# Kernel optimization log

Hardware: AMD Instinct MI355X
Metric: run time of the kernel (lower is better)

## Reference

```python
import jax, jax.numpy as jnp
import numpy as np
from jax import lax


def _sobel3d_kernels():
    # Standard separable 3D Sobel: derivative d=[-1,0,1] along one axis,
    # smoothing s=[1,2,1] along the other two. Axes order (D, H, W).
    d = np.array([-1.0, 0.0, 1.0], dtype=np.float32)
    s = np.array([1.0, 2.0, 1.0], dtype=np.float32)
    kx = np.einsum('i,j,k->ijk', d, s, s)  # derivative along D
    ky = np.einsum('i,j,k->ijk', s, d, s)  # derivative along H
    kz = np.einsum('i,j,k->ijk', s, s, d)  # derivative along W
    # Stack as [Cout=3, Cin=1, 3, 3, 3] -> one conv computes x,y,z grads at once.
    return jnp.asarray(np.stack([kx, ky, kz])[:, None])


_DN = ('NCDHW', 'OIDHW', 'NCDHW')


def _conv3(x, k):
    # x: [N, 1, D, H, W], k: [3, 1, 3, 3, 3] -> [N, 3, D-2, H-2, W-2]
    # torch F.conv3d and lax conv are both cross-correlation; VALID padding.
    return lax.conv_general_dilated(x, k, (1, 1, 1), 'VALID', dimension_numbers=_DN)


def _g2(inp, k):
    # inp: [B, D, H, W, C] (channels last, as the torch module permutes)
    b, dd, hh, ww, c = inp.shape
    x = jnp.transpose(inp, (0, 4, 1, 2, 3)).reshape(b * c, 1, dd, hh, ww)
    g1 = _conv3(x, k)                                  # [B*C, 3, D-2, H-2, W-2]
    mag = jnp.sqrt(jnp.sum(g1 * g1, axis=1, keepdims=True))  # first-order magnitude
    g2 = _conv3(mag, k)                                # [B*C, 3, D-4, H-4, W-4]
    gx, gy, gz = g2[:, 0], g2[:, 1], g2[:, 2]
    # Faithful to source: sqrt(x^2 + y^2) + z^2 (note: z is squared, not inside sqrt)
    out = jnp.sqrt(gx * gx + gy * gy) + gz * gz        # [B*C, D-4, H-4, W-4]
    return out.reshape(b, c, *out.shape[1:])


def setup_inputs() -> dict:
    key = jax.random.key(0)
    k1, k2 = jax.random.split(key)
    pred = jax.random.normal(k1, (2, 64, 64, 64, 32), dtype=jnp.float32)
    hr = jax.random.normal(k2, (2, 64, 64, 64, 32), dtype=jnp.float32)
    return {'pred': pred, 'hr': hr}


def reference(pred, hr):
    k = _sobel3d_kernels()
    return jnp.mean(jnp.abs(_g2(pred, k) - _g2(hr, k)))
```

## Files before the change

### kernel.cpp

```cpp
#include <hip/hip_runtime.h>
#include <hip/hip_fp16.h>


constexpr int BDIM = 256;
constexpr size_t IN_B = 8388608;
constexpr int IN_D = 131072;
constexpr int IN_H = 2048;
constexpr int M = 62;
constexpr int F = 60;
constexpr int C = 32;
constexpr int MROW = M * C;
constexpr size_t MAGSZ = (size_t)M * M * MROW;
constexpr size_t PLANE = (size_t)M * MROW;
constexpr unsigned NPART = 1440;

__device__ __forceinline__ float4 ld4(const float* p) {
    return *reinterpret_cast<const float4*>(p);
}
__device__ __forceinline__ float2 ldh2(const __half* p) {
    return __half22float2(*reinterpret_cast<const __half2*>(p));
}
__device__ __forceinline__ float4 sm3(float4 a, float4 b, float4 c) {
    return make_float4(a.x + 2.f * b.x + c.x, a.y + 2.f * b.y + c.y,
                       a.z + 2.f * b.z + c.z, a.w + 2.f * b.w + c.w);
}
__device__ __forceinline__ float4 df2(float4 a, float4 c) {
    return make_float4(c.x - a.x, c.y - a.y, c.z - a.z, c.w - a.w);
}

struct P1W { float4 A[2], B[2], C[2]; };

__device__ __forceinline__ void p1_plane(const float* __restrict__ col, size_t zoff,
                                         P1W& W)
{
    float4 S[4], D[4];
#pragma unroll
    for (int r = 0; r < 4; ++r) {
        const float* p = col + zoff + (size_t)r * IN_H;
        float4 a = ld4(p), b = ld4(p + C), c = ld4(p + 2 * C);
        S[r] = sm3(a, b, c);
        D[r] = df2(a, c);
    }
#pragma unroll
    for (int k = 0; k < 2; ++k) {
        W.A[k] = sm3(S[k], S[k+1], S[k+2]);
        W.B[k] = df2(S[k], S[k+2]);
        W.C[k] = sm3(D[k], D[k+1], D[k+2]);
    }
}

__device__ __forceinline__ void p1_emit(const P1W& W0, const P1W& W1, const P1W& W2,
                                        __half* __restrict__ mag, size_t cb,
                                        int z, int y0, bool wr)
{
    if (!wr) return;
#pragma unroll
    for (int k = 0; k < 2; ++k) {
        float4 gx = df2(W0.A[k], W2.A[k]);
        float4 gy = sm3(W0.B[k], W1.B[k], W2.B[k]);
        float4 gz = sm3(W0.C[k], W1.C[k], W2.C[k]);
        float mx = sqrtf(gx.x * gx.x + gy.x * gy.x + gz.x * gz.x);
        float my = sqrtf(gx.y * gx.y + gy.y * gy.y + gz.y * gz.y);
        float mz = sqrtf(gx.z * gx.z + gy.z * gy.z + gz.z * gz.z);
        float mw = sqrtf(gx.w * gx.w + gy.w * gy.w + gz.w * gz.w);
        union { __half2 h[2]; float2 f; } u;
        u.h[0] = __floats2half2_rn(mx, my);
        u.h[1] = __floats2half2_rn(mz, mw);
        *reinterpret_cast<float2*>(mag + ((size_t)z * M + (y0 + k)) * MROW + cb)
            = u.f;
    }
}

__global__ __launch_bounds__(BDIM) void sobel_mag_v7(
    const float* __restrict__ pred, const float* __restrict__ hr,
    __half* __restrict__ magP, __half* __restrict__ magH,
    int b, unsigned* __restrict__ counter, int zeroCtr)
{
    if (zeroCtr && blockIdx.x == 0 && blockIdx.y == 0 && blockIdx.z == 0 &&
        threadIdx.x == 0)
        __hip_atomic_store(counter, 0u, __ATOMIC_RELAXED,
                           __HIP_MEMORY_SCOPE_AGENT);

    const int xt = blockIdx.x & 1, yt = blockIdx.x >> 1;
    const int zc = blockIdx.y;
    const float* __restrict__ in  = blockIdx.z ? hr   : pred;
    __half*      __restrict__ mag = blockIdx.z ? magH : magP;

    const int c4 = (threadIdx.x & 7) << 2;
    const int xl = threadIdx.x >> 3;
    const int x0 = xt * 30;
    const int x  = x0 + xl;
    const bool wr = (xt == 0) || (xl >= 2);
    const int y0 = yt * 2;
    const int z0 = zc * 8;
    const int zn = min(8, M - z0);

    const float* col = in + (size_t)b * IN_B + (size_t)y0 * IN_H
                          + (size_t)x * C + c4;
    const size_t cb = (size_t)x * C + c4;

    P1W W0, W1, W2;
    p1_plane(col, (size_t)(z0 + 0) * IN_D, W0);
    p1_plane(col, (size_t)(z0 + 1) * IN_D, W1);
    int z = 0;
    while (true) {
        p1_plane(col, (size_t)(z0 + z + 2) * IN_D, W2);
        p1_emit(W0, W1, W2, mag, cb, z0 + z, y0, wr);
        if (++z >= zn) break;
        p1_plane(col, (size_t)(z0 + z + 2) * IN_D, W0);
        p1_emit(W1, W2, W0, mag, cb, z0 + z, y0, wr);
        if (++z >= zn) break;
        p1_plane(col, (size_t)(z0 + z + 2) * IN_D, W1);
        p1_emit(W2, W0, W1, mag, cb, z0 + z, y0, wr);
        if (++z >= zn) break;
    }
}

struct P2W { float2 A[2], B[2], C[2]; };

__device__ __forceinline__ void p2_plane(const __half* __restrict__ col, size_t zoff,
                                         P2W& W)
{
    float2 SX[4], DX[4];
#pragma unroll
    for (int j = 0; j < 4; ++j) {
        const __half* p = col + zoff + (size_t)j * MROW;
        float2 a = ldh2(p), b = ldh2(p + C), c = ldh2(p + 2 * C);
        SX[j] = make_float2(a.x + 2.f * b.x + c.x, a.y + 2.f * b.y + c.y);
        DX[j] = make_float2(c.x - a.x, c.y - a.y);
    }
#pragma unroll
    for (int k = 0; k < 2; ++k) {
        W.A[k] = make_float2(SX[k].x + 2.f * SX[k+1].x + SX[k+2].x,
                             SX[k].y + 2.f * SX[k+1].y + SX[k+2].y);
        W.B[k] = make_float2(SX[k+2].x - SX[k].x, SX[k+2].y - SX[k].y);
        W.C[k] = make_float2(DX[k].x + 2.f * DX[k+1].x + DX[k+2].x,
                             DX[k].y + 2.f * DX[k+1].y + DX[k+2].y);
    }
}

__device__ __forceinline__ void p2_emit(const P2W& P0, const P2W& P1, const P2W& P2,
                                        const P2W& H0, const P2W& H1, const P2W& H2,
                                        float& acc)
{
#pragma unroll
    for (int k = 0; k < 2; ++k) {
        float gxPx = P2.A[k].x - P0.A[k].x;
        float gxPy = P2.A[k].y - P0.A[k].y;
        float gyPx = P0.B[k].x + 2.f * P1.B[k].x + P2.B[k].x;
        float gyPy = P0.B[k].y + 2.f * P1.B[k].y + P2.B[k].y;
        float gzPx = P0.C[k].x + 2.f * P1.C[k].x + P2.C[k].x;
        float gzPy = P0.C[k].y + 2.f * P1.C[k].y + P2.C[k].y;
        float gxHx = H2.A[k].x - H0.A[k].x;
        float gxHy = H2.A[k].y - H0.A[k].y;
        float gyHx = H0.B[k].x + 2.f * H1.B[k].x + H2.B[k].x;
        float gyHy = H0.B[k].y + 2.f * H1.B[k].y + H2.B[k].y;
        float gzHx = H0.C[k].x + 2.f * H1.C[k].x + H2.C[k].x;
        float gzHy = H0.C[k].y + 2.f * H1.C[k].y + H2.C[k].y;
        float oPx = sqrtf(gxPx * gxPx + gyPx * gyPx) + gzPx * gzPx;
        float oPy = sqrtf(gxPy * gxPy + gyPy * gyPy) + gzPy * gzPy;
        float oHx = sqrtf(gxHx * gxHx + gyHx * gyHx) + gzHx * gzHx;
        float oHy = sqrtf(gxHy * gxHy + gyHy * gyHy) + gzHy * gzHy;
        acc += fabsf(oPx - oHx) + fabsf(oPy - oHy);
    }
}

__global__ __launch_bounds__(BDIM) void sobel2_v7(
    const __half* __restrict__ magP, const __half* __restrict__ magH,
    int b, float* __restrict__ partial, unsigned* __restrict__ counter,
    float* __restrict__ out)
{
    const int xt = blockIdx.x & 3, yt = blockIdx.x >> 2;
    const int zc = blockIdx.y;
    const int y0 = yt * 2;
    const int z0 = zc * 10;
    const int xraw = xt * 16 + (threadIdx.x >> 4);
    const bool xok = xraw < F;
    const int x = min(xraw, F - 1);
    const int c2 = (threadIdx.x & 15) << 1;

    const size_t colo = (size_t)y0 * MROW + (size_t)x * C + c2;
    const __half* colP = magP + colo;
    const __half* colH = magH + colo;

    P2W P0, P1, P2, H0, H1, H2;
    p2_plane(colP, (size_t)(z0 + 0) * PLANE, P0);
    p2_plane(colH, (size_t)(z0 + 0) * PLANE, H0);
    p2_plane(colP, (size_t)(z0 + 1) * PLANE, P1);
    p2_plane(colH, (size_t)(z0 + 1) * PLANE, H1);
    float acc = 0.f;
    int z = 0;
    while (true) {
        p2_plane(colP, (size_t)(z0 + z + 2) * PLANE, P2);
        p2_plane(colH, (size_t)(z0 + z + 2) * PLANE, H2);
        if (xok) p2_emit(P0, P1, P2, H0, H1, H2, acc);
        if (++z >= 10) break;
        p2_plane(colP, (size_t)(z0 + z + 2) * PLANE, P0);
        p2_plane(colH, (size_t)(z0 + z + 2) * PLANE, H0);
        if (xok) p2_emit(P1, P2, P0, H1, H2, H0, acc);
        if (++z >= 10) break;
        p2_plane(colP, (size_t)(z0 + z + 2) * PLANE, P1);
        p2_plane(colH, (size_t)(z0 + z + 2) * PLANE, H1);
        if (xok) p2_emit(P2, P0, P1, H2, H0, H1, acc);
        if (++z >= 10) break;
    }

    for (int o = 32; o > 0; o >>= 1) acc += __shfl_down(acc, o, 64);
    __shared__ float sred[BDIM / 64];
    __shared__ int isLast;
    const int lane = threadIdx.x & 63, wv = threadIdx.x >> 6;
    if (lane == 0) sred[wv] = acc;
    __syncthreads();
    if (threadIdx.x == 0) {
        float t = 0.f;
#pragma unroll
        for (int i = 0; i < BDIM / 64; ++i) t += sred[i];
        const size_t pidx = (size_t)b * 720 + (size_t)zc * 120 + blockIdx.x;
        __hip_atomic_store(&partial[pidx], t, __ATOMIC_RELAXED,
                           __HIP_MEMORY_SCOPE_AGENT);
        const unsigned old = __hip_atomic_fetch_add(counter, 1u, __ATOMIC_ACQ_REL,
                                                    __HIP_MEMORY_SCOPE_AGENT);
        isLast = (old == NPART - 1u) ? 1 : 0;
    }
    __syncthreads();

    if (isLast) {
        double a = 0.0;
        for (unsigned i = threadIdx.x; i < NPART; i += BDIM)
            a += (double)__hip_atomic_load(&partial[i], __ATOMIC_RELAXED,
                                           __HIP_MEMORY_SCOPE_AGENT);
        for (int o = 32; o > 0; o >>= 1) a += __shfl_down(a, o, 64);
        __shared__ double sd[BDIM / 64];
        if (lane == 0) sd[wv] = a;
        __syncthreads();
        if (threadIdx.x == 0) {
            double t = 0.0;
#pragma unroll
            for (int i = 0; i < BDIM / 64; ++i) t += sd[i];
            out[0] = (float)(t / 13824000.0);
        }
    }
}

extern "C" void kernel_launch(void* const* d_in, const int* in_sizes, int n_in,
                              void* d_out, int out_size, void* d_ws, size_t ws_size,
                              hipStream_t stream)
{
    const float* pred = (const float*)d_in[0];
    const float* hr   = (const float*)d_in[1];

    float* partial = (float*)d_ws;
    unsigned* counter = (unsigned*)((char*)d_ws + 32768);
    __half* magP = (__half*)((char*)d_ws + 65536);
    __half* magH = magP + MAGSZ;

    for (int b = 0; b < 2; ++b) {
        sobel_mag_v7<<<dim3(62, 8, 2), BDIM, 0, stream>>>(
            pred, hr, magP, magH, b, counter, b == 0 ? 1 : 0);
        sobel2_v7<<<dim3(120, 6), BDIM, 0, stream>>>(
            magP, magH, b, partial, counter, (float*)d_out);
    }
}
```

Before: 257.5 us.

## Stage input planes through LDS with async global_load_lds double buffering

Both stencil kernels now stream each z-plane into shared memory with asynchronous global-to-LDS DMA loads, double-buffered and fenced by explicit vmcnt waits and barriers. Threads then read their neighbouring x values from LDS instead of issuing overlapping global loads. The magnitude buffer gets a padded row pitch, the first kernel covers a full x row per block, and the second kernel switches to 4-wide half vectors with a new grid shape and partial count. This aims to cut redundant global traffic and hide load latency, at the cost of 64KB of LDS per block in the first kernel (lowering occupancy) and hand-tuned wait counts that are easy to get wrong.

```diff
diff --git a/kernel.cpp b/kernel.cpp
--- a/kernel.cpp
+++ b/kernel.cpp
@@ -8,17 +8,38 @@
 constexpr int IN_H = 2048;
 constexpr int M = 62;
 constexpr int F = 60;
-constexpr int C = 32;
-constexpr int MROW = M * C;
-constexpr size_t MAGSZ = (size_t)M * M * MROW;
-constexpr size_t PLANE = (size_t)M * MROW;
-constexpr unsigned NPART = 1440;
+constexpr int PMROW = 2048;
+constexpr size_t PPLANE = (size_t)M * PMROW;
+constexpr size_t PMAGSZ = (size_t)M * PPLANE;
+constexpr unsigned NPART = 1800;
+
+__device__ __forceinline__ void dma16(const void* g, void* l) {
+    __builtin_amdgcn_global_load_lds(
+        (const __attribute__((address_space(1))) void*)g,
+        (__attribute__((address_space(3))) void*)l, 16, 0, 0);
+}
+
+#define WAITBAR(N) do { \
+    asm volatile("s_waitcnt vmcnt(" #N ")" ::: "memory"); \
+    __builtin_amdgcn_sched_barrier(0); \
+    __builtin_amdgcn_s_barrier(); \
+    __builtin_amdgcn_sched_barrier(0); \
+} while (0)
+
+#define MIDBAR() do { \
+    __builtin_amdgcn_sched_barrier(0); \
+    __builtin_amdgcn_s_barrier(); \
+    __builtin_amdgcn_sched_barrier(0); \
+} while (0)
 
 __device__ __forceinline__ float4 ld4(const float* p) {
     return *reinterpret_cast<const float4*>(p);
 }
-__device__ __forceinline__ float2 ldh2(const __half* p) {
-    return __half22float2(*reinterpret_cast<const __half2*>(p));
+__device__ __forceinline__ float4 ldh4(const __half* p) {
+    float2 r = *reinterpret_cast<const float2*>(p);
+    const __half2* h = reinterpret_cast<const __half2*>(&r);
+    float2 lo = __half22float2(h[0]), hi = __half22float2(h[1]);
+    return make_float4(lo.x, lo.y, hi.x, hi.y);
 }
 __device__ __forceinline__ float4 sm3(float4 a, float4 b, float4 c) {
     return make_float4(a.x + 2.f * b.x + c.x, a.y + 2.f * b.y + c.y,
@@ -30,14 +51,14 @@
 
 struct P1W { float4 A[2], B[2], C[2]; };
 
-__device__ __forceinline__ void p1_plane(const float* __restrict__ col, size_t zoff,
-                                         P1W& W)
+__device__ __forceinline__ void p1_partials(const float* __restrict__ sb,
+                                            int x, int c4, P1W& W)
 {
     float4 S[4], D[4];
 #pragma unroll
     for (int r = 0; r < 4; ++r) {
-        const float* p = col + zoff + (size_t)r * IN_H;
-        float4 a = ld4(p), b = ld4(p + C), c = ld4(p + 2 * C);
+        const float* p = sb + r * 2048 + x * 32 + c4;
+        float4 a = ld4(p), b = ld4(p + 32), c = ld4(p + 64);
         S[r] = sm3(a, b, c);
         D[r] = df2(a, c);
     }
@@ -49,191 +70,246 @@
     }
 }
 
-__device__ __forceinline__ void p1_emit(const P1W& W0, const P1W& W1, const P1W& W2,
-                                        __half* __restrict__ mag, size_t cb,
-                                        int z, int y0, bool wr)
-{
-    if (!wr) return;
+__device__ __forceinline__ void p1_emit4(const P1W& W0, const P1W& W1, const P1W& W2,
+                                         __half* __restrict__ mag, int x, int c4,
+                                         int z, int y0)
+{
 #pragma unroll
     for (int k = 0; k < 2; ++k) {
         float4 gx = df2(W0.A[k], W2.A[k]);
         float4 gy = sm3(W0.B[k], W1.B[k], W2.B[k]);
         float4 gz = sm3(W0.C[k], W1.C[k], W2.C[k]);
-        float mx = sqrtf(gx.x * gx.x + gy.x * gy.x + gz.x * gz.x);
-        float my = sqrtf(gx.y * gx.y + gy.y * gy.y + gz.y * gz.y);
-        float mz = sqrtf(gx.z * gx.z + gy.z * gy.z + gz.z * gz.z);
-        float mw = sqrtf(gx.w * gx.w + gy.w * gy.w + gz.w * gz.w);
+        float m0 = sqrtf(gx.x * gx.x + gy.x * gy.x + gz.x * gz.x);
+        float m1 = sqrtf(gx.y * gx.y + gy.y * gy.y + gz.y * gz.y);
+        float m2 = sqrtf(gx.z * gx.z + gy.z * gy.z + gz.z * gz.z);
+        float m3 = sqrtf(gx.w * gx.w + gy.w * gy.w + gz.w * gz.w);
         union { __half2 h[2]; float2 f; } u;
-        u.h[0] = __floats2half2_rn(mx, my);
-        u.h[1] = __floats2half2_rn(mz, mw);
-        *reinterpret_cast<float2*>(mag + ((size_t)z * M + (y0 + k)) * MROW + cb)
-            = u.f;
-    }
-}
-
-__global__ __launch_bounds__(BDIM) void sobel_mag_v7(
+        u.h[0] = __floats2half2_rn(m0, m1);
+        u.h[1] = __floats2half2_rn(m2, m3);
+        *reinterpret_cast<float2*>(
+            mag + (size_t)z * PPLANE + (size_t)(y0 + k) * PMROW + x * 32 + c4) = u.f;
+    }
+}
+
+__global__ __launch_bounds__(BDIM) void sobel_mag_v8(
     const float* __restrict__ pred, const float* __restrict__ hr,
     __half* __restrict__ magP, __half* __restrict__ magH,
     int b, unsigned* __restrict__ counter, int zeroCtr)
 {
+    __shared__ char smem[65536];
+
     if (zeroCtr && blockIdx.x == 0 && blockIdx.y == 0 && blockIdx.z == 0 &&
         threadIdx.x == 0)
         __hip_atomic_store(counter, 0u, __ATOMIC_RELAXED,
                            __HIP_MEMORY_SCOPE_AGENT);
 
-    const int xt = blockIdx.x & 1, yt = blockIdx.x >> 1;
+    const int yt = blockIdx.x;
     const int zc = blockIdx.y;
     const float* __restrict__ in  = blockIdx.z ? hr   : pred;
     __half*      __restrict__ mag = blockIdx.z ? magH : magP;
-
-    const int c4 = (threadIdx.x & 7) << 2;
-    const int xl = threadIdx.x >> 3;
-    const int x0 = xt * 30;
-    const int x  = x0 + xl;
-    const bool wr = (xt == 0) || (xl >= 2);
     const int y0 = yt * 2;
     const int z0 = zc * 8;
     const int zn = min(8, M - z0);
-
-    const float* col = in + (size_t)b * IN_B + (size_t)y0 * IN_H
-                          + (size_t)x * C + c4;
-    const size_t cb = (size_t)x * C + c4;
-
-    P1W W0, W1, W2;
-    p1_plane(col, (size_t)(z0 + 0) * IN_D, W0);
-    p1_plane(col, (size_t)(z0 + 1) * IN_D, W1);
+    const int tid = threadIdx.x;
+    const int c4 = (tid & 7) << 2;
+    const int xA = tid >> 3;
+    const int xB = xA + 32;
+    const bool xBok = xB < M;
+
+    const char* gIn = (const char*)in +
+        ((size_t)b * IN_B + (size_t)y0 * IN_H) * 4 + (size_t)tid * 16;
+
+    auto ISSUE = [&](int q, int zz) {
+        const char* g = gIn + (size_t)min(zz, 63) * (IN_D * 4);
+        char* l = smem + q * 32768 + tid * 16;
+#pragma unroll
+        for (int k = 0; k < 8; ++k)
+            dma16(g + k * 4096, l + k * 4096);
+    };
+
+    P1W A0, A1, A2, B0, B1, B2;
+    auto COMPA = [&](int q, P1W& Wa, P1W& Wb) {
+        const float* sb = (const float*)(smem + q * 32768);
+        p1_partials(sb, xA, c4, Wa);
+        if (xBok) p1_partials(sb, xB, c4, Wb);
+    };
+
+    ISSUE(0, z0 + 0); ISSUE(1, z0 + 1);
+    WAITBAR(8);
+    COMPA(0, A0, B0);
+    MIDBAR(); ISSUE(0, z0 + 2);
+    WAITBAR(8);
+    COMPA(1, A1, B1);
+    MIDBAR(); ISSUE(1, z0 + 3);
+
     int z = 0;
     while (true) {
-        p1_plane(col, (size_t)(z0 + z + 2) * IN_D, W2);
-        p1_emit(W0, W1, W2, mag, cb, z0 + z, y0, wr);
+        WAITBAR(8);
+        COMPA(z & 1, A2, B2);
+        p1_emit4(A0, A1, A2, mag, xA, c4, z0 + z, y0);
+        if (xBok) p1_emit4(B0, B1, B2, mag, xB, c4, z0 + z, y0);
+        MIDBAR(); ISSUE(z & 1, z0 + z + 4);
         if (++z >= zn) break;
-        p1_plane(col, (size_t)(z0 + z + 2) * IN_D, W0);
-        p1_emit(W1, W2, W0, mag, cb, z0 + z, y0, wr);
+        WAITBAR(8);
+        COMPA(z & 1, A0, B0);
+        p1_emit4(A1, A2, A0, mag, xA, c4, z0 + z, y0);
+        if (xBok) p1_emit4(B1, B2, B0, mag, xB, c4, z0 + z, y0);
+        MIDBAR(); ISSUE(z & 1, z0 + z + 4);
         if (++z >= zn) break;
-        p1_plane(col, (size_t)(z0 + z + 2) * IN_D, W1);
-        p1_emit(W2, W0, W1, mag, cb, z0 + z, y0, wr);
+        WAITBAR(8);
+        COMPA(z & 1, A1, B1);
+        p1_emit4(A2, A0, A1, mag, xA, c4, z0 + z, y0);
+        if (xBok) p1_emit4(B2, B0, B1, mag, xB, c4, z0 + z, y0);
+        MIDBAR(); ISSUE(z & 1, z0 + z + 4);
         if (++z >= zn) break;
     }
-}
-
-struct P2W { float2 A[2], B[2], C[2]; };
-
-__device__ __forceinline__ void p2_plane(const __half* __restrict__ col, size_t zoff,
-                                         P2W& W)
-{
-    float2 SX[4], DX[4];
+    asm volatile("s_waitcnt vmcnt(0)" ::: "memory");
+}
+
+struct P2W4 { float4 A[2], B[2], C[2]; };
+
+__device__ __forceinline__ void p2_partials(const __half* __restrict__ sb,
+                                            int xl, int c4, P2W4& W)
+{
+    float4 S[4], D[4];
 #pragma unroll
     for (int j = 0; j < 4; ++j) {
-        const __half* p = col + zoff + (size_t)j * MROW;
-        float2 a = ldh2(p), b = ldh2(p + C), c = ldh2(p + 2 * C);
-        SX[j] = make_float2(a.x + 2.f * b.x + c.x, a.y + 2.f * b.y + c.y);
-        DX[j] = make_float2(c.x - a.x, c.y - a.y);
+        const __half* p = sb + j * 1024 + xl * 32 + c4;
+        float4 a = ldh4(p), b = ldh4(p + 32), c = ldh4(p + 64);
+        S[j] = sm3(a, b, c);
+        D[j] = df2(a, c);
     }
 #pragma unroll
     for (int k = 0; k < 2; ++k) {
-        W.A[k] = make_float2(SX[k].x + 2.f * SX[k+1].x + SX[k+2].x,
-                             SX[k].y + 2.f * SX[k+1].y + SX[k+2].y);
-        W.B[k] = make_float2(SX[k+2].x - SX[k].x, SX[k+2].y - SX[k].y);
-        W.C[k] = make_float2(DX[k].x + 2.f * DX[k+1].x + DX[k+2].x,
-                             DX[k].y + 2.f * DX[k+1].y + DX[k+2].y);
-    }
-}
-
-__device__ __forceinline__ void p2_emit(const P2W& P0, const P2W& P1, const P2W& P2,
-                                        const P2W& H0, const P2W& H1, const P2W& H2,
-                                        float& acc)
+        W.A[k] = sm3(S[k], S[k+1], S[k+2]);
+        W.B[k] = df2(S[k], S[k+2]);
+        W.C[k] = sm3(D[k], D[k+1], D[k+2]);
+    }
+}
+
+__device__ __forceinline__ void p2_emit4(const P2W4& P0, const P2W4& P1, const P2W4& P2,
+                                         const P2W4& H0, const P2W4& H1, const P2W4& H2,
+                                         float& acc)
 {
 #pragma unroll
     for (int k = 0; k < 2; ++k) {
-        float gxPx = P2.A[k].x - P0.A[k].x;
-        float gxPy = P2.A[k].y - P0.A[k].y;
-        float gyPx = P0.B[k].x + 2.f * P1.B[k].x + P2.B[k].x;
-        float gyPy = P0.B[k].y + 2.f * P1.B[k].y + P2.B[k].y;
-        float gzPx = P0.C[k].x + 2.f * P1.C[k].x + P2.C[k].x;
-        float gzPy = P0.C[k].y + 2.f * P1.C[k].y + P2.C[k].y;
-        float gxHx = H2.A[k].x - H0.A[k].x;
-        float gxHy = H2.A[k].y - H0.A[k].y;
-        float gyHx = H0.B[k].x + 2.f * H1.B[k].x + H2.B[k].x;
-        float gyHy = H0.B[k].y + 2.f * H1.B[k].y + H2.B[k].y;
-        float gzHx = H0.C[k].x + 2.f * H1.C[k].x + H2.C[k].x;
-        float gzHy = H0.C[k].y + 2.f * H1.C[k].y + H2.C[k].y;
-        float oPx = sqrtf(gxPx * gxPx + gyPx * gyPx) + gzPx * gzPx;
-        float oPy = sqrtf(gxPy * gxPy + gyPy * gyPy) + gzPy * gzPy;
-        float oHx = sqrtf(gxHx * gxHx + gyHx * gyHx) + gzHx * gzHx;
-        float oHy = sqrtf(gxHy * gxHy + gyHy * gyHy) + gzHy * gzHy;
-        acc += fabsf(oPx - oHx) + fabsf(oPy - oHy);
-    }
-}
-
-__global__ __launch_bounds__(BDIM) void sobel2_v7(
+        float4 gxP = df2(P0.A[k], P2.A[k]);
+        float4 gyP = sm3(P0.B[k], P1.B[k], P2.B[k]);
+        float4 gzP = sm3(P0.C[k], P1.C[k], P2.C[k]);
+        float4 gxH = df2(H0.A[k], H2.A[k]);
+        float4 gyH = sm3(H0.B[k], H1.B[k], H2.B[k]);
+        float4 gzH = sm3(H0.C[k], H1.C[k], H2.C[k]);
+        acc += fabsf((sqrtf(gxP.x*gxP.x + gyP.x*gyP.x) + gzP.x*gzP.x)
+                   - (sqrtf(gxH.x*gxH.x + gyH.x*gyH.x) + gzH.x*gzH.x));
+        acc += fabsf((sqrtf(gxP.y*gxP.y + gyP.y*gyP.y) + gzP.y*gzP.y)
+                   - (sqrtf(gxH.y*gxH.y + gyH.y*gyH.y) + gzH.y*gzH.y));
+        acc += fabsf((sqrtf(gxP.z*gxP.z + gyP.z*gyP.z) + gzP.z*gzP.z)
+                   - (sqrtf(gxH.z*gxH.z + gyH.z*gyH.z) + gzH.z*gzH.z));
+        acc += fabsf((sqrtf(gxP.w*gxP.w + gyP.w*gyP.w) + gzP.w*gzP.w)
+                   - (sqrtf(gxH.w*gxH.w + gyH.w*gyH.w) + gzH.w*gzH.w));
+    }
+}
+
+__global__ __launch_bounds__(BDIM) void sobel2_v8(
     const __half* __restrict__ magP, const __half* __restrict__ magH,
     int b, float* __restrict__ partial, unsigned* __restrict__ counter,
     float* __restrict__ out)
 {
-    const int xt = blockIdx.x & 3, yt = blockIdx.x >> 2;
+    __shared__ char smem[32768];
+
+    const int xt = blockIdx.x & 1, yt = blockIdx.x >> 1;
     const int zc = blockIdx.y;
+    const int x0 = xt * 30;
     const int y0 = yt * 2;
-    const int z0 = zc * 10;
-    const int xraw = xt * 16 + (threadIdx.x >> 4);
-    const bool xok = xraw < F;
-    const int x = min(xraw, F - 1);
-    const int c2 = (threadIdx.x & 15) << 1;
-
-    const size_t colo = (size_t)y0 * MROW + (size_t)x * C + c2;
-    const __half* colP = magP + colo;
-    const __half* colH = magH + colo;
-
-    P2W P0, P1, P2, H0, H1, H2;
-    p2_plane(colP, (size_t)(z0 + 0) * PLANE, P0);
-    p2_plane(colH, (size_t)(z0 + 0) * PLANE, H0);
-    p2_plane(colP, (size_t)(z0 + 1) * PLANE, P1);
-    p2_plane(colH, (size_t)(z0 + 1) * PLANE, H1);
+    const int z0 = zc * 4;
+    const int tid = threadIdx.x;
+    const int c4 = (tid & 7) << 2;
+    const int xl = tid >> 3;
+    const bool xok = xl < 30;
+
+    const char* gPbase = (const char*)magP + (size_t)y0 * 4096 + (size_t)x0 * 64;
+    const char* gHbase = (const char*)magH + (size_t)y0 * 4096 + (size_t)x0 * 64;
+    const int sub = tid >> 7;
+    const int off = (tid & 127) * 16;
+
+    auto ISSUE = [&](int q, int zz) {
+        const size_t pb = (size_t)min(zz, M - 1) * (PPLANE * 2);
+        const char* gP = gPbase + pb;
+        const char* gH = gHbase + pb;
+        char* lb = smem + q * 16384;
+        const int j0 = sub, j1 = 2 + sub;
+        dma16(gP + (size_t)j0 * 4096 + off, lb + j0 * 2048 + off);
+        dma16(gP + (size_t)j1 * 4096 + off, lb + j1 * 2048 + off);
+        dma16(gH + (size_t)j0 * 4096 + off, lb + 8192 + j0 * 2048 + off);
+        dma16(gH + (size_t)j1 * 4096 + off, lb + 8192 + j1 * 2048 + off);
+    };
+
+    P2W4 P0, P1, P2, H0, H1, H2;
+    auto COMP = [&](int q, P2W4& P, P2W4& H) {
+        if (!xok) return;
+        const __half* sb = (const __half*)(smem + q * 16384);
+        p2_partials(sb,        xl, c4, P);
+        p2_partials(sb + 4096, xl, c4, H);
+    };
+
     float acc = 0.f;
-    int z = 0;
-    while (true) {
-        p2_plane(colP, (size_t)(z0 + z + 2) * PLANE, P2);
-        p2_plane(colH, (size_t)(z0 + z + 2) * PLANE, H2);
-        if (xok) p2_emit(P0, P1, P2, H0, H1, H2, acc);
-        if (++z >= 10) break;
-        p2_plane(colP, (size_t)(z0 + z + 2) * PLANE, P0);
-        p2_plane(colH, (size_t)(z0 + z + 2) * PLANE, H0);
-        if (xok) p2_emit(P1, P2, P0, H1, H2, H0, acc);
-        if (++z >= 10) break;
-        p2_plane(colP, (size_t)(z0 + z + 2) * PLANE, P1);
-        p2_plane(colH, (size_t)(z0 + z + 2) * PLANE, H1);
-        if (xok) p2_emit(P2, P0, P1, H2, H0, H1, acc);
-        if (++z >= 10) break;
-    }
+
+    ISSUE(0, z0 + 0); ISSUE(1, z0 + 1);
+    WAITBAR(4);
+    COMP(0, P0, H0);
+    MIDBAR(); ISSUE(0, z0 + 2);
+    WAITBAR(4);
+    COMP(1, P1, H1);
+    MIDBAR(); ISSUE(1, z0 + 3);
+
+    WAITBAR(4);
+    COMP(0, P2, H2);
+    if (xok) p2_emit4(P0, P1, P2, H0, H1, H2, acc);
+    MIDBAR(); ISSUE(0, z0 + 4);
+    WAITBAR(4);
+    COMP(1, P0, H0);
+    if (xok) p2_emit4(P1, P2, P0, H1, H2, H0, acc);
+    MIDBAR(); ISSUE(1, z0 + 5);
+    WAITBAR(4);
+    COMP(0, P1, H1);
+    if (xok) p2_emit4(P2, P0, P1, H2, H0, H1, acc);
+    MIDBAR(); ISSUE(0, z0 + 6);
+    WAITBAR(4);
+    COMP(1, P2, H2);
+    if (xok) p2_emit4(P0, P1, P2, H0, H1, H2, acc);
+
+    asm volatile("s_waitcnt vmcnt(0)" ::: "memory");
+    __syncthreads();
 
     for (int o = 32; o > 0; o >>= 1) acc += __shfl_down(acc, o, 64);
-    __shared__ float sred[BDIM / 64];
-    __shared__ int isLast;
-    const int lane = threadIdx.x & 63, wv = threadIdx.x >> 6;
+    float* sred = (float*)smem;
+    int* isLast = (int*)(smem + 64);
+    double* sd = (double*)(smem + 128);
+    const int lane = tid & 63, wv = tid >> 6;
     if (lane == 0) sred[wv] = acc;
     __syncthreads();
-    if (threadIdx.x == 0) {
+    if (tid == 0) {
         float t = 0.f;
 #pragma unroll
         for (int i = 0; i < BDIM / 64; ++i) t += sred[i];
-        const size_t pidx = (size_t)b * 720 + (size_t)zc * 120 + blockIdx.x;
+        const size_t pidx = (size_t)b * 900 + (size_t)zc * 60 + blockIdx.x;
         __hip_atomic_store(&partial[pidx], t, __ATOMIC_RELAXED,
                            __HIP_MEMORY_SCOPE_AGENT);
         const unsigned old = __hip_atomic_fetch_add(counter, 1u, __ATOMIC_ACQ_REL,
                                                     __HIP_MEMORY_SCOPE_AGENT);
-        isLast = (old == NPART - 1u) ? 1 : 0;
+        *isLast = (old == NPART - 1u) ? 1 : 0;
     }
     __syncthreads();
 
-    if (isLast) {
+    if (*isLast) {
         double a = 0.0;
-        for (unsigned i = threadIdx.x; i < NPART; i += BDIM)
+        for (unsigned i = tid; i < NPART; i += BDIM)
             a += (double)__hip_atomic_load(&partial[i], __ATOMIC_RELAXED,
                                            __HIP_MEMORY_SCOPE_AGENT);
         for (int o = 32; o > 0; o >>= 1) a += __shfl_down(a, o, 64);
-        __shared__ double sd[BDIM / 64];
         if (lane == 0) sd[wv] = a;
         __syncthreads();
-        if (threadIdx.x == 0) {
+        if (tid == 0) {
             double t = 0.0;
 #pragma unroll
             for (int i = 0; i < BDIM / 64; ++i) t += sd[i];
@@ -252,12 +328,12 @@
     float* partial = (float*)d_ws;
     unsigned* counter = (unsigned*)((char*)d_ws + 32768);
     __half* magP = (__half*)((char*)d_ws + 65536);
-    __half* magH = magP + MAGSZ;
+    __half* magH = magP + PMAGSZ;
 
     for (int b = 0; b < 2; ++b) {
-        sobel_mag_v7<<<dim3(62, 8, 2), BDIM, 0, stream>>>(
+        sobel_mag_v8<<<dim3(31, 8, 2), BDIM, 0, stream>>>(
             pred, hr, magP, magH, b, counter, b == 0 ? 1 : 0);
-        sobel2_v7<<<dim3(120, 6), BDIM, 0, stream>>>(
+        sobel2_v8<<<dim3(60, 15), BDIM, 0, stream>>>(
             magP, magH, b, partial, counter, (float*)d_out);
     }
 }
```

New measurement: 279.0 us. 1.08x slower.

## Fuse both Sobel passes into one persistent cooperative kernel with grid sync

Applied to the files above, without the earlier changes.

Replaces the four launches (two per batch) with a single cooperative kernel of 512 persistent blocks. Each block loops over first-pass work units for both batches, waits at a grid-wide sync, then loops over second-pass units, and ends with one final reduction. The aim is to cut launch gaps and let both batches run together, at the cost of a larger magnitude workspace and a grid barrier. The old multi-launch path is kept as a fallback if the workspace is too small or the cooperative launch fails.

```diff
diff --git a/kernel.cpp b/kernel.cpp
--- a/kernel.cpp
+++ b/kernel.cpp
@@ -1,8 +1,12 @@
 #include <hip/hip_runtime.h>
 #include <hip/hip_fp16.h>
+#include <hip/hip_cooperative_groups.h>
+
+namespace cg = cooperative_groups;
 
 
 constexpr int BDIM = 256;
+constexpr int NB   = 512;
 constexpr size_t IN_B = 8388608;
 constexpr int IN_D = 131072;
 constexpr int IN_H = 2048;
@@ -12,7 +16,6 @@
 constexpr int MROW = M * C;
 constexpr size_t MAGSZ = (size_t)M * M * MROW;
 constexpr size_t PLANE = (size_t)M * MROW;
-constexpr unsigned NPART = 1440;
 
 __device__ __forceinline__ float4 ld4(const float* p) {
     return *reinterpret_cast<const float4*>(p);
@@ -59,37 +62,26 @@
         float4 gx = df2(W0.A[k], W2.A[k]);
         float4 gy = sm3(W0.B[k], W1.B[k], W2.B[k]);
         float4 gz = sm3(W0.C[k], W1.C[k], W2.C[k]);
-        float mx = sqrtf(gx.x * gx.x + gy.x * gy.x + gz.x * gz.x);
-        float my = sqrtf(gx.y * gx.y + gy.y * gy.y + gz.y * gz.y);
-        float mz = sqrtf(gx.z * gx.z + gy.z * gy.z + gz.z * gz.z);
-        float mw = sqrtf(gx.w * gx.w + gy.w * gy.w + gz.w * gz.w);
+        float m0 = sqrtf(gx.x * gx.x + gy.x * gy.x + gz.x * gz.x);
+        float m1 = sqrtf(gx.y * gx.y + gy.y * gy.y + gz.y * gz.y);
+        float m2 = sqrtf(gx.z * gx.z + gy.z * gy.z + gz.z * gz.z);
+        float m3 = sqrtf(gx.w * gx.w + gy.w * gy.w + gz.w * gz.w);
         union { __half2 h[2]; float2 f; } u;
-        u.h[0] = __floats2half2_rn(mx, my);
-        u.h[1] = __floats2half2_rn(mz, mw);
+        u.h[0] = __floats2half2_rn(m0, m1);
+        u.h[1] = __floats2half2_rn(m2, m3);
         *reinterpret_cast<float2*>(mag + ((size_t)z * M + (y0 + k)) * MROW + cb)
             = u.f;
     }
 }
 
-__global__ __launch_bounds__(BDIM) void sobel_mag_v7(
-    const float* __restrict__ pred, const float* __restrict__ hr,
-    __half* __restrict__ magP, __half* __restrict__ magH,
-    int b, unsigned* __restrict__ counter, int zeroCtr)
-{
-    if (zeroCtr && blockIdx.x == 0 && blockIdx.y == 0 && blockIdx.z == 0 &&
-        threadIdx.x == 0)
-        __hip_atomic_store(counter, 0u, __ATOMIC_RELAXED,
-                           __HIP_MEMORY_SCOPE_AGENT);
-
-    const int xt = blockIdx.x & 1, yt = blockIdx.x >> 1;
-    const int zc = blockIdx.y;
-    const float* __restrict__ in  = blockIdx.z ? hr   : pred;
-    __half*      __restrict__ mag = blockIdx.z ? magH : magP;
-
-    const int c4 = (threadIdx.x & 7) << 2;
-    const int xl = threadIdx.x >> 3;
-    const int x0 = xt * 30;
-    const int x  = x0 + xl;
+__device__ __forceinline__ void p1_unit(const float* __restrict__ in,
+                                        __half* __restrict__ mag,
+                                        int b, int bx, int zc, int tid)
+{
+    const int xt = bx & 1, yt = bx >> 1;
+    const int c4 = (tid & 7) << 2;
+    const int xl = tid >> 3;
+    const int x  = xt * 30 + xl;
     const bool wr = (xt == 0) || (xl >= 2);
     const int y0 = yt * 2;
     const int z0 = zc * 8;
@@ -165,19 +157,17 @@
     }
 }
 
-__global__ __launch_bounds__(BDIM) void sobel2_v7(
-    const __half* __restrict__ magP, const __half* __restrict__ magH,
-    int b, float* __restrict__ partial, unsigned* __restrict__ counter,
-    float* __restrict__ out)
-{
-    const int xt = blockIdx.x & 3, yt = blockIdx.x >> 2;
-    const int zc = blockIdx.y;
+__device__ __forceinline__ void p2_unit(const __half* __restrict__ magP,
+                                        const __half* __restrict__ magH,
+                                        int bx, int zc, int tid, float& acc)
+{
+    const int xt = bx & 3, yt = bx >> 2;
     const int y0 = yt * 2;
     const int z0 = zc * 10;
-    const int xraw = xt * 16 + (threadIdx.x >> 4);
+    const int xraw = xt * 16 + (tid >> 4);
     const bool xok = xraw < F;
     const int x = min(xraw, F - 1);
-    const int c2 = (threadIdx.x & 15) << 1;
+    const int c2 = (tid & 15) << 1;
 
     const size_t colo = (size_t)y0 * MROW + (size_t)x * C + c2;
     const __half* colP = magP + colo;
@@ -188,7 +178,6 @@
     p2_plane(colH, (size_t)(z0 + 0) * PLANE, H0);
     p2_plane(colP, (size_t)(z0 + 1) * PLANE, P1);
     p2_plane(colH, (size_t)(z0 + 1) * PLANE, H1);
-    float acc = 0.f;
     int z = 0;
     while (true) {
         p2_plane(colP, (size_t)(z0 + z + 2) * PLANE, P2);
@@ -204,36 +193,40 @@
         if (xok) p2_emit(P2, P0, P1, H2, H0, H1, acc);
         if (++z >= 10) break;
     }
-
+}
+
+__device__ __forceinline__ void tail_reduce(float acc, float* __restrict__ partial,
+                                            size_t pidx, unsigned* __restrict__ counter,
+                                            unsigned npart, float* __restrict__ out,
+                                            int tid)
+{
     for (int o = 32; o > 0; o >>= 1) acc += __shfl_down(acc, o, 64);
     __shared__ float sred[BDIM / 64];
     __shared__ int isLast;
-    const int lane = threadIdx.x & 63, wv = threadIdx.x >> 6;
+    __shared__ double sd[BDIM / 64];
+    const int lane = tid & 63, wv = tid >> 6;
     if (lane == 0) sred[wv] = acc;
     __syncthreads();
-    if (threadIdx.x == 0) {
+    if (tid == 0) {
         float t = 0.f;
 #pragma unroll
         for (int i = 0; i < BDIM / 64; ++i) t += sred[i];
-        const size_t pidx = (size_t)b * 720 + (size_t)zc * 120 + blockIdx.x;
         __hip_atomic_store(&partial[pidx], t, __ATOMIC_RELAXED,
                            __HIP_MEMORY_SCOPE_AGENT);
         const unsigned old = __hip_atomic_fetch_add(counter, 1u, __ATOMIC_ACQ_REL,
                                                     __HIP_MEMORY_SCOPE_AGENT);
-        isLast = (old == NPART - 1u) ? 1 : 0;
+        isLast = (old == npart - 1u) ? 1 : 0;
     }
     __syncthreads();
-
     if (isLast) {
         double a = 0.0;
-        for (unsigned i = threadIdx.x; i < NPART; i += BDIM)
+        for (unsigned i = tid; i < npart; i += BDIM)
             a += (double)__hip_atomic_load(&partial[i], __ATOMIC_RELAXED,
                                            __HIP_MEMORY_SCOPE_AGENT);
         for (int o = 32; o > 0; o >>= 1) a += __shfl_down(a, o, 64);
-        __shared__ double sd[BDIM / 64];
         if (lane == 0) sd[wv] = a;
         __syncthreads();
-        if (threadIdx.x == 0) {
+        if (tid == 0) {
             double t = 0.0;
 #pragma unroll
             for (int i = 0; i < BDIM / 64; ++i) t += sd[i];
@@ -242,22 +235,98 @@
     }
 }
 
+__global__ __launch_bounds__(BDIM, 2) void sobel_fused(
+    const float* __restrict__ pred, const float* __restrict__ hr,
+    __half* __restrict__ magBase, float* __restrict__ partial,
+    unsigned* __restrict__ counter, float* __restrict__ out)
+{
+    const int tid = threadIdx.x;
+    if (blockIdx.x == 0 && tid == 0)
+        __hip_atomic_store(counter, 0u, __ATOMIC_RELAXED,
+                           __HIP_MEMORY_SCOPE_AGENT);
+
+    for (int u = blockIdx.x; u < 1984; u += NB) {
+        const int bx = u % 62;
+        int r = u / 62;
+        const int zc  = r & 7;  r >>= 3;
+        const int inp = r & 1;
+        const int b   = r >> 1;
+        const float* in = inp ? hr : pred;
+        __half* mag = magBase + ((size_t)b * 2 + inp) * MAGSZ;
+        p1_unit(in, mag, b, bx, zc, tid);
+    }
+
+    cg::this_grid().sync();
+
+    float acc = 0.f;
+    for (int u = blockIdx.x; u < 1440; u += NB) {
+        const int bx = u % 120;
+        int r = u / 120;
+        const int zc = r % 6;
+        const int b  = r / 6;
+        const __half* mP = magBase + ((size_t)b * 2 + 0) * MAGSZ;
+        const __half* mH = magBase + ((size_t)b * 2 + 1) * MAGSZ;
+        p2_unit(mP, mH, bx, zc, tid, acc);
+    }
+
+    tail_reduce(acc, partial, blockIdx.x, counter, NB, out, tid);
+}
+
+__global__ __launch_bounds__(BDIM) void sobel_mag_v9(
+    const float* __restrict__ pred, const float* __restrict__ hr,
+    __half* __restrict__ magP, __half* __restrict__ magH,
+    int b, unsigned* __restrict__ counter, int zeroCtr)
+{
+    if (zeroCtr && blockIdx.x == 0 && blockIdx.y == 0 && blockIdx.z == 0 &&
+        threadIdx.x == 0)
+        __hip_atomic_store(counter, 0u, __ATOMIC_RELAXED,
+                           __HIP_MEMORY_SCOPE_AGENT);
+    const float* in = blockIdx.z ? hr : pred;
+    __half* mag = blockIdx.z ? magH : magP;
+    p1_unit(in, mag, b, blockIdx.x, blockIdx.y, threadIdx.x);
+}
+
+__global__ __launch_bounds__(BDIM) void sobel2_v9(
+    const __half* __restrict__ magP, const __half* __restrict__ magH,
+    int b, float* __restrict__ partial, unsigned* __restrict__ counter,
+    float* __restrict__ out)
+{
+    float acc = 0.f;
+    p2_unit(magP, magH, blockIdx.x, blockIdx.y, threadIdx.x, acc);
+    const size_t pidx = (size_t)b * 720 + (size_t)blockIdx.y * 120 + blockIdx.x;
+    tail_reduce(acc, partial, pidx, counter, 1440u, out, (int)threadIdx.x);
+}
+
 extern "C" void kernel_launch(void* const* d_in, const int* in_sizes, int n_in,
                               void* d_out, int out_size, void* d_ws, size_t ws_size,
                               hipStream_t stream)
 {
     const float* pred = (const float*)d_in[0];
     const float* hr   = (const float*)d_in[1];
-
-    float* partial = (float*)d_ws;
+    float* outp       = (float*)d_out;
+
+    float* partial    = (float*)d_ws;
     unsigned* counter = (unsigned*)((char*)d_ws + 32768);
-    __half* magP = (__half*)((char*)d_ws + 65536);
-    __half* magH = magP + MAGSZ;
-
-    for (int b = 0; b < 2; ++b) {
-        sobel_mag_v7<<<dim3(62, 8, 2), BDIM, 0, stream>>>(
-            pred, hr, magP, magH, b, counter, b == 0 ? 1 : 0);
-        sobel2_v7<<<dim3(120, 6), BDIM, 0, stream>>>(
-            magP, magH, b, partial, counter, (float*)d_out);
-    }
-}
+    __half* magBase   = (__half*)((char*)d_ws + 65536);
+
+    const size_t need4 = 65536 + 4 * MAGSZ * sizeof(__half);
+
+    bool done = false;
+    if (ws_size >= need4) {
+        void* args[] = { (void*)&pred, (void*)&hr, (void*)&magBase,
+                         (void*)&partial, (void*)&counter, (void*)&outp };
+        done = hipLaunchCooperativeKernel((const void*)sobel_fused,
+                                          dim3(NB), dim3(BDIM), args, 0,
+                                          stream) == hipSuccess;
+    }
+    if (!done) {
+        __half* magP = magBase;
+        __half* magH = magBase + MAGSZ;
+        for (int b = 0; b < 2; ++b) {
+            sobel_mag_v9<<<dim3(62, 8, 2), BDIM, 0, stream>>>(
+                pred, hr, magP, magH, b, counter, b == 0 ? 1 : 0);
+            sobel2_v9<<<dim3(120, 6), BDIM, 0, stream>>>(
+                magP, magH, b, partial, counter, outp);
+        }
+    }
+}
```

After: 320.6 us. +24.5%, slower.
